# Kernel optimization log

Measured on AMD Instinct MI355X. Metric: run time of the kernel, lower is better.

The kernel has to match this reference:

```python
import jax, jax.numpy as jnp
import numpy as np

L, B, N, D, H, INTER = 4, 64, 128, 1024, 16, 4096
HD = D // H
EPS = 1e-12


def layer_norm(x, g, b):
    m = jnp.mean(x, axis=-1, keepdims=True)
    v = jnp.mean(jnp.square(x - m), axis=-1, keepdims=True)
    return (x - m) * jax.lax.rsqrt(v + EPS) * g + b


def fast_self_attention(x, wq_w, wq_b, wk_w, wk_b, hwq, hwk, tr_w, tr_b):
    # x: [B, T, D]
    Bq, T, _ = x.shape
    q = x @ wq_w + wq_b                                  # [B,T,D]
    hq = q.reshape(Bq, T, H, HD).transpose(0, 2, 1, 3)    # [B,H,T,hd]
    # additive attention over queries (mask scores are all-zero here)
    alpha = jax.nn.softmax(jnp.einsum('bhtd,hd->bht', hq, hwq) / np.sqrt(HD), axis=-1)
    gq = jnp.einsum('bht,bhtd->bhd', alpha, hq).reshape(Bq, 1, D)  # global query [B,1,D]
    k = x @ wk_w + wk_b
    p = k * gq                                            # [B,T,D]
    hp = p.reshape(Bq, T, H, HD).transpose(0, 2, 1, 3)
    beta = jax.nn.softmax(jnp.einsum('bhtd,hd->bht', hp, hwk) / np.sqrt(HD), axis=-1)
    gk = jnp.einsum('bht,bhtd->bhd', beta, hp).reshape(Bq, 1, D)   # global key [B,1,D]
    u = q * gk
    r = u @ tr_w + tr_b
    return r + q


def encoder_layer(x, p, i):
    a = fast_self_attention(x, p['wq_w'][i], p['wq_b'][i], p['wk_w'][i], p['wk_b'][i],
                            p['hwq'][i], p['hwk'][i], p['tr_w'][i], p['tr_b'][i])
    a = a @ p['so_w'][i] + p['so_b'][i]
    a = layer_norm(a, p['ln1_g'][i], p['ln1_b'][i])
    h = jax.nn.gelu(a @ p['int_w'][i] + p['int_b'][i], approximate=False)
    o = h @ p['out_w'][i] + p['out_b'][i]
    return layer_norm(o + a, p['ln2_g'][i], p['ln2_b'][i])


def setup_inputs() -> dict:
    key = jax.random.key(0)
    ks = iter(jax.random.split(key, 32))
    s = 0.02
    inp = {
        'x': jax.random.normal(next(ks), (B, N, D), jnp.float32),
        'wq_w': jax.random.normal(next(ks), (L, D, D)) * s,
        'wq_b': jnp.zeros((L, D)),
        'wk_w': jax.random.normal(next(ks), (L, D, D)) * s,
        'wk_b': jnp.zeros((L, D)),
        'hwq': jax.random.normal(next(ks), (L, H, HD)) * s,
        'hwk': jax.random.normal(next(ks), (L, H, HD)) * s,
        'tr_w': jax.random.normal(next(ks), (L, D, D)) * s,
        'tr_b': jnp.zeros((L, D)),
        'so_w': jax.random.normal(next(ks), (L, D, D)) * s,
        'so_b': jnp.zeros((L, D)),
        'ln1_g': jnp.ones((L, D)),
        'ln1_b': jnp.zeros((L, D)),
        'int_w': jax.random.normal(next(ks), (L, D, INTER)) * s,
        'int_b': jnp.zeros((L, INTER)),
        'out_w': jax.random.normal(next(ks), (L, INTER, D)) * s,
        'out_b': jnp.zeros((L, D)),
        'ln2_g': jnp.ones((L, D)),
        'ln2_b': jnp.zeros((L, D)),
        'pool_w': jax.random.normal(next(ks), (D, D)) * s,
        'pool_b': jnp.zeros((D,)),
        'pool_q': jax.random.normal(next(ks), (D,)) * s,
    }
    return inp


def reference(x, wq_w, wq_b, wk_w, wk_b, hwq, hwk, tr_w, tr_b, so_w, so_b,
              ln1_g, ln1_b, int_w, int_b, out_w, out_b, ln2_g, ln2_b,
              pool_w, pool_b, pool_q):
    p = dict(wq_w=wq_w, wq_b=wq_b, wk_w=wk_w, wk_b=wk_b, hwq=hwq, hwk=hwk,
             tr_w=tr_w, tr_b=tr_b, so_w=so_w, so_b=so_b, ln1_g=ln1_g, ln1_b=ln1_b,
             int_w=int_w, int_b=int_b, out_w=out_w, out_b=out_b, ln2_g=ln2_g, ln2_b=ln2_b)
    h = x
    for i in range(L):
        h = encoder_layer(h, p, i)
    # additive attention pooling (mask scores are zeros)
    scores = jnp.tanh(h @ pool_w + pool_b) @ pool_q       # [B,N]
    w = jax.nn.softmax(scores, axis=-1)
    return jnp.einsum('bn,bnd->bd', w, h)                 # [B,D]
```

## Files before the change

### kernel.cpp

```cpp
#include <hip/hip_runtime.h>
#include <hip/hip_bf16.h>
#include <math.h>

typedef unsigned short u16;
typedef __attribute__((ext_vector_type(4))) unsigned short u16x4;
typedef __attribute__((ext_vector_type(8))) unsigned short u16x8;
typedef __attribute__((ext_vector_type(8))) short s16x8;
typedef __attribute__((ext_vector_type(4))) float f32x4;

typedef const __attribute__((address_space(1))) void* gas_t;
typedef __attribute__((address_space(3))) void* las_t;

#define DI __device__ __forceinline__

static constexpr int Bc = 64, Nc = 128, Dc = 1024, Hc = 16, HDc = 64, Ic = 4096, Lc = 4;
static constexpr int Mrows = Bc * Nc;

DI float b2f(u16 u) { union { unsigned i; float f; } x; x.i = ((unsigned)u) << 16; return x.f; }
DI u16 f2b(float f) {
  union { float f; unsigned i; } x; x.f = f;
  unsigned r = x.i + 0x7FFF + ((x.i >> 16) & 1);
  return (u16)(r >> 16);
}

#define BARRIER do { asm volatile("" ::: "memory"); __builtin_amdgcn_s_barrier(); asm volatile("" ::: "memory"); } while (0)
#define VMC(N) asm volatile("s_waitcnt vmcnt(" #N ")" ::: "memory")

#define STG(PTR, ROW0, T, SLOT) do { \
    const u16* _s = (PTR) + (size_t)((ROW0) + srow) * K + (((T) << 6) + scol); \
    __builtin_amdgcn_global_load_lds((gas_t)_s, (las_t)(smem + (SLOT) + ldsw), 16, 0, 0); \
    __builtin_amdgcn_global_load_lds((gas_t)(_s + ((size_t)K << 3)), (las_t)(smem + (SLOT) + ldsw + 1024), 16, 0, 0); \
  } while (0)

#define LDA(BUFB, RH) do { \
    _Pragma("unroll") \
    for (int mi = 0; mi < 4; ++mi) { \
      af[mi][0] = *(const s16x8*)(smem + (BUFB) + Abase_rd + (RH) * 8192 + mi * 2048 + aoff0); \
      af[mi][1] = *(const s16x8*)(smem + (BUFB) + Abase_rd + (RH) * 8192 + mi * 2048 + aoff1); \
    } } while (0)

#define LDB(DST, BUFB, CH) do { \
    _Pragma("unroll") \
    for (int nj = 0; nj < 2; ++nj) { \
      DST[nj][0] = *(const s16x8*)(smem + (BUFB) + Bbase_rd + (CH) * 4096 + nj * 2048 + aoff0); \
      DST[nj][1] = *(const s16x8*)(smem + (BUFB) + Bbase_rd + (CH) * 4096 + nj * 2048 + aoff1); \
    } } while (0)

#define MFMAQ(RH, CH, BF) do { \
    __builtin_amdgcn_s_setprio(1); \
    _Pragma("unroll") \
    for (int kk = 0; kk < 2; ++kk) \
      _Pragma("unroll") \
      for (int mi = 0; mi < 4; ++mi) \
        _Pragma("unroll") \
        for (int nj = 0; nj < 2; ++nj) \
          acc[(RH) * 4 + mi][(CH) * 2 + nj] = __builtin_amdgcn_mfma_f32_16x16x32_bf16( \
              af[mi][kk], BF[nj][kk], acc[(RH) * 4 + mi][(CH) * 2 + nj], 0, 0, 0); \
    __builtin_amdgcn_s_setprio(0); \
  } while (0)

template <int EPI, bool SPLIT>
__global__ __launch_bounds__(512, 2) void gemm256(
    const u16* __restrict__ A, const u16* __restrict__ BT,
    const float* __restrict__ bias, const float* __restrict__ bias2,
    const u16* __restrict__ resid, u16* __restrict__ C, u16* __restrict__ C2,
    int M, int N, int K, int NC) {
  extern __shared__ __align__(16) char smem[];
  const int tid = threadIdx.x;
  const int l = tid & 63;
  const int w = tid >> 6;
  const int wr = w >> 2, wc = w & 3;

  const int GX = gridDim.x;
  int wg = blockIdx.y * GX + blockIdx.x;
  const int nwg = GX * gridDim.y;
  wg = (wg & 7) * (nwg >> 3) + (wg >> 3);
  const int bn0 = (wg % GX) * 256;
  const int bm0 = (wg / GX) * 256;

  const int NT = K >> 6;
  const int NI = NT >> 1;

  const int row_l = l & 15;
  const int kl = (l >> 4) * 8;
  const int xr = (row_l & 7) << 3;
  const int aoff0 = row_l * 128 + (((0 * 32 + kl) ^ xr) * 2);
  const int aoff1 = row_l * 128 + (((1 * 32 + kl) ^ xr) * 2);
  const int Abase_rd = wr * 16384;
  const int Bbase_rd = 32768 + (wc >> 1) * 16384 + (wc & 1) * 8192;

  const int srow = w * 16 + (l >> 3);
  const int scol = ((l & 7) ^ ((l >> 3) & 7)) << 3;
  const int ldsw = w * 2048;

  enum { b0A0 = 0, b0A1 = 16384, b0B0 = 32768, b0B1 = 49152,
         b1A0 = 65536, b1A1 = 81920, b1B0 = 98304, b1B1 = 114688 };

  STG(BT, bn0, 0, b0B0);
  STG(BT, bn0 + 128, 0, b0B1);
  STG(A, bm0, 0, b0A0);
  STG(A, bm0 + 128, 0, b0A1);
  STG(BT, bn0, 1, b1B0);
  STG(BT, bn0 + 128, 1, b1B1);
  VMC(4);
  BARRIER;

  f32x4 acc[8][4];
#pragma unroll
  for (int i = 0; i < 8; ++i)
#pragma unroll
    for (int j = 0; j < 4; ++j) acc[i][j] = f32x4{0.f, 0.f, 0.f, 0.f};
  s16x8 af[4][2], bf0[2][2], bf1[2][2];

  for (int j = 0; j < NI; ++j) {
    const int t1 = 2 * j + 1;
    int t2 = 2 * j + 2; if (t2 >= NT) t2 = 0;
    int t3 = 2 * j + 3; if (t3 >= NT) t3 = 1;
    LDA(0, 0); LDB(bf0, 0, 0);
    STG(A, bm0, t1, b1A0);
    BARRIER; MFMAQ(0, 0, bf0); BARRIER;
    LDB(bf1, 0, 1);
    STG(A, bm0 + 128, t1, b1A1);
    BARRIER; MFMAQ(0, 1, bf1); BARRIER;
    LDA(0, 1);
    STG(BT, bn0, t2, b0B0);
    BARRIER; MFMAQ(1, 0, bf0); BARRIER;
    STG(BT, bn0 + 128, t2, b0B1);
    STG(A, bm0, t2, b0A0);
    VMC(6);
    BARRIER; MFMAQ(1, 1, bf1); BARRIER;
    LDA(65536, 0); LDB(bf0, 65536, 0);
    STG(A, bm0 + 128, t2, b0A1);
    BARRIER; MFMAQ(0, 0, bf0); BARRIER;
    LDB(bf1, 65536, 1);
    BARRIER; MFMAQ(0, 1, bf1); BARRIER;
    LDA(65536, 1);
    STG(BT, bn0, t3, b1B0);
    BARRIER; MFMAQ(1, 0, bf0); BARRIER;
    STG(BT, bn0 + 128, t3, b1B1);
    VMC(4);
    BARRIER; MFMAQ(1, 1, bf1); BARRIER;
  }

  u16* Cout = C;
  const float* bi = bias;
  int cb = bn0;
  if (SPLIT) {
    const int half = N >> 1;
    if (bn0 >= half) { Cout = C2; bi = bias2; cb = bn0 - half; }
  }
  const int r0 = bm0 + wr * 128 + ((l >> 4) << 2);
#pragma unroll
  for (int fi = 0; fi < 8; ++fi) {
#pragma unroll
    for (int fj = 0; fj < 4; ++fj) {
      const int ocol = cb + wc * 64 + fj * 16 + (l & 15);
      const float bv = bi[ocol];
      const int row = r0 + fi * 16;
#pragma unroll
      for (int r = 0; r < 4; ++r) {
        float v = acc[fi][fj][r] + bv;
        if constexpr (EPI == 1) v += b2f(resid[(size_t)(row + r) * NC + ocol]);
        if constexpr (EPI == 2) v = 0.5f * v * (1.f + erff(v * 0.70710678118654752f));
        if constexpr (EPI == 3) v = tanhf(v);
        Cout[(size_t)(row + r) * NC + ocol] = f2b(v);
      }
    }
  }
}

#define LDA2(BUFB, RH) do { \
    _Pragma("unroll") \
    for (int mi = 0; mi < 2; ++mi) { \
      af[mi][0] = *(const s16x8*)(smem + (BUFB) + Abase_rd + ((RH) * 2 + mi) * 2048 + aoff0); \
      af[mi][1] = *(const s16x8*)(smem + (BUFB) + Abase_rd + ((RH) * 2 + mi) * 2048 + aoff1); \
    } } while (0)

#define MFMAQ2(RH, CH, BF) do { \
    __builtin_amdgcn_s_setprio(1); \
    _Pragma("unroll") \
    for (int kk = 0; kk < 2; ++kk) \
      _Pragma("unroll") \
      for (int mi = 0; mi < 2; ++mi) \
        _Pragma("unroll") \
        for (int nj = 0; nj < 2; ++nj) \
          acc[(RH) * 2 + mi][(CH) * 2 + nj] = __builtin_amdgcn_mfma_f32_16x16x32_bf16( \
              af[mi][kk], BF[nj][kk], acc[(RH) * 2 + mi][(CH) * 2 + nj], 0, 0, 0); \
    __builtin_amdgcn_s_setprio(0); \
  } while (0)

template <int EPI>
__global__ __launch_bounds__(512, 2) void gemm128n(
    const u16* __restrict__ A, const u16* __restrict__ BT,
    const float* __restrict__ bias, const u16* __restrict__ resid,
    u16* __restrict__ C, int M, int N, int K, int NC) {
  extern __shared__ __align__(16) char smem[];
  const int tid = threadIdx.x;
  const int l = tid & 63;
  const int w = tid >> 6;
  const int wr = w >> 1, wc = w & 1;

  const int GX = gridDim.x;
  int wg = blockIdx.y * GX + blockIdx.x;
  const int nwg = GX * gridDim.y;
  wg = (wg & 7) * (nwg >> 3) + (wg >> 3);
  const int bn0 = (wg % GX) * 128;
  const int bm0 = (wg / GX) * 256;

  const int NT = K >> 6;
  const int NI = NT >> 1;

  const int row_l = l & 15;
  const int kl = (l >> 4) * 8;
  const int xr = (row_l & 7) << 3;
  const int aoff0 = row_l * 128 + (((0 * 32 + kl) ^ xr) * 2);
  const int aoff1 = row_l * 128 + (((1 * 32 + kl) ^ xr) * 2);
  const int Abase_rd = (wr >> 1) * 16384 + (wr & 1) * 8192;
  const int Bbase_rd = 32768 + wc * 8192;

  const int srow = w * 16 + (l >> 3);
  const int scol = ((l & 7) ^ ((l >> 3) & 7)) << 3;
  const int ldsw = w * 2048;

  enum { c0A0 = 0, c0A1 = 16384, c0B = 32768,
         c1A0 = 49152, c1A1 = 65536, c1B = 81920 };

  STG(BT, bn0, 0, c0B);
  STG(A, bm0, 0, c0A0);
  STG(A, bm0 + 128, 0, c0A1);
  STG(BT, bn0, 1, c1B);
  VMC(2);
  BARRIER;

  f32x4 acc[4][4];
#pragma unroll
  for (int i = 0; i < 4; ++i)
#pragma unroll
    for (int j = 0; j < 4; ++j) acc[i][j] = f32x4{0.f, 0.f, 0.f, 0.f};
  s16x8 af[2][2], bf0[2][2], bf1[2][2];

  for (int j = 0; j < NI; ++j) {
    const int t1 = 2 * j + 1;
    int t2 = 2 * j + 2; if (t2 >= NT) t2 = 0;
    int t3 = 2 * j + 3; if (t3 >= NT) t3 = 1;
    LDA2(0, 0); LDB(bf0, 0, 0);
    STG(A, bm0, t1, c1A0);
    BARRIER; MFMAQ2(0, 0, bf0); BARRIER;
    LDB(bf1, 0, 1);
    STG(A, bm0 + 128, t1, c1A1);
    BARRIER; MFMAQ2(0, 1, bf1); BARRIER;
    LDA2(0, 1);
    STG(BT, bn0, t2, c0B);
    BARRIER; MFMAQ2(1, 0, bf0); BARRIER;
    STG(A, bm0, t2, c0A0);
    VMC(4);
    BARRIER; MFMAQ2(1, 1, bf1); BARRIER;
    LDA2(49152, 0); LDB(bf0, 49152, 0);
    STG(A, bm0 + 128, t2, c0A1);
    BARRIER; MFMAQ2(0, 0, bf0); BARRIER;
    LDB(bf1, 49152, 1);
    BARRIER; MFMAQ2(0, 1, bf1); BARRIER;
    LDA2(49152, 1);
    STG(BT, bn0, t3, c1B);
    BARRIER; MFMAQ2(1, 0, bf0); BARRIER;
    VMC(2);
    BARRIER; MFMAQ2(1, 1, bf1); BARRIER;
  }

  const int r0 = bm0 + wr * 64 + ((l >> 4) << 2);
#pragma unroll
  for (int fi = 0; fi < 4; ++fi) {
#pragma unroll
    for (int fj = 0; fj < 4; ++fj) {
      const int ocol = bn0 + wc * 64 + fj * 16 + (l & 15);
      const float bv = bias[ocol];
      const int row = r0 + fi * 16;
#pragma unroll
      for (int r = 0; r < 4; ++r) {
        float v = acc[fi][fj][r] + bv;
        if constexpr (EPI == 1) v += b2f(resid[(size_t)(row + r) * NC + ocol]);
        if constexpr (EPI == 2) v = 0.5f * v * (1.f + erff(v * 0.70710678118654752f));
        if constexpr (EPI == 3) v = tanhf(v);
        C[(size_t)(row + r) * NC + ocol] = f2b(v);
      }
    }
  }
}

DI void ttile(const float* in, u16* out, int R, int C, int r0, int c0, int t) {
  __shared__ u16 tile[32][33];
  const int lr = t >> 3;
  const int lc = (t & 7) * 4;
  f32x4 v = *(const f32x4*)(in + (size_t)(r0 + lr) * C + c0 + lc);
#pragma unroll
  for (int j = 0; j < 4; ++j) tile[lr][lc + j] = f2b(v[j]);
  __syncthreads();
  u16x4 o;
#pragma unroll
  for (int j = 0; j < 4; ++j) o[j] = tile[lc + j][lr];
  *(u16x4*)(out + (size_t)(c0 + lr) * R + r0 + lc) = o;
}

__global__ __launch_bounds__(256) void transpose_cvt(
    const float* __restrict__ in, u16* __restrict__ out, int R, int C) {
  ttile(in, out, R, C, blockIdx.y * 32, blockIdx.x * 32, threadIdx.x);
}

__global__ __launch_bounds__(256) void transpose4sq(
    const float* s0, const float* s1, const float* s2, const float* s3,
    u16* d0, u16* d1, u16* d2, u16* d3) {
  const int z = blockIdx.z;
  const float* in = z == 0 ? s0 : z == 1 ? s1 : z == 2 ? s2 : s3;
  u16* out = z == 0 ? d0 : z == 1 ? d1 : z == 2 ? d2 : d3;
  ttile(in, out, 1024, 1024, blockIdx.y * 32, blockIdx.x * 32, threadIdx.x);
}

__global__ __launch_bounds__(256) void transpose_io(
    const float* si, u16* di, const float* so, u16* dout) {
  if (blockIdx.z == 0) {
    ttile(si, di, 1024, 4096, blockIdx.y * 32, blockIdx.x * 32, threadIdx.x);
  } else {
    ttile(so, dout, 4096, 1024, blockIdx.x * 32, blockIdx.y * 32, threadIdx.x);
  }
}

__global__ __launch_bounds__(256) void cvt_k(
    const float* __restrict__ in, u16* __restrict__ out) {
  const size_t i = ((size_t)blockIdx.x * 256 + threadIdx.x) * 8;
  f32x4 a = *(const f32x4*)(in + i);
  f32x4 b = *(const f32x4*)(in + i + 4);
  u16x8 o;
#pragma unroll
  for (int j = 0; j < 4; ++j) o[j] = f2b(a[j]);
#pragma unroll
  for (int j = 0; j < 4; ++j) o[4 + j] = f2b(b[j]);
  *(u16x8*)(out + i) = o;
}

__global__ __launch_bounds__(128) void attn_gq(
    const u16* __restrict__ q, const float* __restrict__ hwq, float* __restrict__ gq) {
  const int bh = blockIdx.x;
  const int b = bh >> 4, h = bh & 15;
  const int tid = threadIdx.x;
  const int lane = tid & 63, wv = tid >> 6;
  __shared__ float hw[64];
  __shared__ float ex[128];
  __shared__ float part[64];
  __shared__ float xw[4];
  if (tid < 64) hw[tid] = hwq[h * 64 + tid];
  __syncthreads();
  const u16* row = q + ((size_t)(b * 128 + tid)) * Dc + h * 64;
  float s = 0.f;
#pragma unroll
  for (int c = 0; c < 8; ++c) {
    u16x8 v = *(const u16x8*)(row + c * 8);
#pragma unroll
    for (int j = 0; j < 8; ++j) s += b2f(v[j]) * hw[c * 8 + j];
  }
  s *= 0.125f;
  float m = s;
  for (int o = 32; o; o >>= 1) m = fmaxf(m, __shfl_xor(m, o));
  if (lane == 0) xw[wv] = m;
  __syncthreads();
  m = fmaxf(xw[0], xw[1]);
  const float e = __expf(s - m);
  ex[tid] = e;
  float sm = e;
  for (int o = 32; o; o >>= 1) sm += __shfl_xor(sm, o);
  if (lane == 0) xw[2 + wv] = sm;
  __syncthreads();
  const float sum = xw[2] + xw[3];
  const int d = tid & 63, half = tid >> 6;
  const u16* colp = q + ((size_t)(b * 128 + half * 64)) * Dc + h * 64 + d;
  float acc = 0.f;
  for (int t = 0; t < 64; ++t) acc += ex[half * 64 + t] * b2f(colp[(size_t)t * Dc]);
  if (half == 0) part[d] = acc;
  __syncthreads();
  if (half == 1) gq[b * Dc + h * 64 + d] = (part[d] + acc) / sum;
}

__global__ __launch_bounds__(128) void attn_gk(
    const u16* __restrict__ k, const float* __restrict__ hwk,
    const float* __restrict__ gq, float* __restrict__ gk) {
  const int bh = blockIdx.x;
  const int b = bh >> 4, h = bh & 15;
  const int tid = threadIdx.x;
  const int lane = tid & 63, wv = tid >> 6;
  __shared__ float hw[64];
  __shared__ float gqv[64];
  __shared__ float ex[128];
  __shared__ float part[64];
  __shared__ float xw[4];
  if (tid < 64) {
    hw[tid] = hwk[h * 64 + tid];
    gqv[tid] = gq[b * Dc + h * 64 + tid];
  }
  __syncthreads();
  const u16* row = k + ((size_t)(b * 128 + tid)) * Dc + h * 64;
  float s = 0.f;
#pragma unroll
  for (int c = 0; c < 8; ++c) {
    u16x8 v = *(const u16x8*)(row + c * 8);
#pragma unroll
    for (int j = 0; j < 8; ++j) s += b2f(v[j]) * gqv[c * 8 + j] * hw[c * 8 + j];
  }
  s *= 0.125f;
  float m = s;
  for (int o = 32; o; o >>= 1) m = fmaxf(m, __shfl_xor(m, o));
  if (lane == 0) xw[wv] = m;
  __syncthreads();
  m = fmaxf(xw[0], xw[1]);
  const float e = __expf(s - m);
  ex[tid] = e;
  float sm = e;
  for (int o = 32; o; o >>= 1) sm += __shfl_xor(sm, o);
  if (lane == 0) xw[2 + wv] = sm;
  __syncthreads();
  const float sum = xw[2] + xw[3];
  const int d = tid & 63, half = tid >> 6;
  const u16* colp = k + ((size_t)(b * 128 + half * 64)) * Dc + h * 64 + d;
  float acc = 0.f;
  for (int t = 0; t < 64; ++t) acc += ex[half * 64 + t] * b2f(colp[(size_t)t * Dc]);
  acc *= gqv[d];
  if (half == 0) part[d] = acc;
  __syncthreads();
  if (half == 1) gk[b * Dc + h * 64 + d] = (part[d] + acc) / sum;
}

__global__ __launch_bounds__(256) void mul_gk(
    const u16* __restrict__ q, const float* __restrict__ gk, u16* __restrict__ u) {
  const size_t i = ((size_t)blockIdx.x * 256 + threadIdx.x) * 8;
  const int col = (int)(i & (Dc - 1));
  const int b = (int)(i >> 17);
  u16x8 v = *(const u16x8*)(q + i);
  const float* g = gk + b * Dc + col;
  u16x8 o;
#pragma unroll
  for (int j = 0; j < 8; ++j) o[j] = f2b(b2f(v[j]) * g[j]);
  *(u16x8*)(u + i) = o;
}

__global__ __launch_bounds__(256) void ln_k(
    const u16* __restrict__ in, const float* __restrict__ g,
    const float* __restrict__ bta, u16* __restrict__ out) {
  const int row = blockIdx.x, tid = threadIdx.x;
  const int lane = tid & 63, wave = tid >> 6;
  __shared__ float red[8];
  const u16* p = in + (size_t)row * Dc + tid * 4;
  u16x4 v = *(const u16x4*)p;
  float x[4];
  float s = 0.f, sq = 0.f;
#pragma unroll
  for (int j = 0; j < 4; ++j) {
    x[j] = b2f(v[j]);
    s += x[j];
    sq += x[j] * x[j];
  }
  for (int o = 32; o; o >>= 1) {
    s += __shfl_down(s, o);
    sq += __shfl_down(sq, o);
  }
  if (lane == 0) {
    red[wave] = s;
    red[4 + wave] = sq;
  }
  __syncthreads();
  s = red[0] + red[1] + red[2] + red[3];
  sq = red[4] + red[5] + red[6] + red[7];
  const float mean = s * (1.f / 1024.f);
  const float var = sq * (1.f / 1024.f) - mean * mean;
  const float rs = rsqrtf(var + 1e-12f);
  f32x4 gv = *(const f32x4*)(g + tid * 4);
  f32x4 bv = *(const f32x4*)(bta + tid * 4);
  u16x4 o;
#pragma unroll
  for (int j = 0; j < 4; ++j) o[j] = f2b((x[j] - mean) * rs * gv[j] + bv[j]);
  *(u16x4*)(out + (size_t)row * Dc + tid * 4) = o;
}

__global__ __launch_bounds__(256) void pool_k(
    const u16* __restrict__ s1, const float* __restrict__ pq,
    const u16* __restrict__ h, float* __restrict__ out) {
  const int b = blockIdx.x, tid = threadIdx.x;
  __shared__ float pqs[1024];
  __shared__ float sc[128];
  __shared__ float ex[128];
  for (int i = tid; i < 1024; i += 256) pqs[i] = pq[i];
  __syncthreads();
  if (tid < 128) {
    const u16* row = s1 + ((size_t)(b * 128 + tid)) * Dc;
    float s = 0.f;
    for (int c = 0; c < 128; ++c) {
      u16x8 v = *(const u16x8*)(row + c * 8);
#pragma unroll
      for (int j = 0; j < 8; ++j) s += b2f(v[j]) * pqs[c * 8 + j];
    }
    sc[tid] = s;
  }
  __syncthreads();
  float m = -1e30f;
  for (int t = 0; t < 128; ++t) m = fmaxf(m, sc[t]);
  if (tid < 128) ex[tid] = __expf(sc[tid] - m);
  __syncthreads();
  float sum = 0.f;
  for (int t = 0; t < 128; ++t) sum += ex[t];
  const int d0 = tid * 4;
  float acc[4] = {0.f, 0.f, 0.f, 0.f};
  for (int n = 0; n < 128; ++n) {
    const float w = ex[n];
    u16x4 v = *(const u16x4*)(h + ((size_t)(b * 128 + n)) * Dc + d0);
#pragma unroll
    for (int j = 0; j < 4; ++j) acc[j] += w * b2f(v[j]);
  }
  const float inv = 1.f / sum;
  f32x4 o;
#pragma unroll
  for (int j = 0; j < 4; ++j) o[j] = acc[j] * inv;
  *(f32x4*)(out + b * Dc + d0) = o;
}

extern "C" void kernel_launch(void* const* d_in, const int* in_sizes, int n_in,
                              void* d_out, int out_size, void* d_ws, size_t ws_size,
                              hipStream_t stream) {
  const float* x = (const float*)d_in[0];
  const float* wq_w = (const float*)d_in[1];
  const float* wq_b = (const float*)d_in[2];
  const float* wk_w = (const float*)d_in[3];
  const float* wk_b = (const float*)d_in[4];
  const float* hwq = (const float*)d_in[5];
  const float* hwk = (const float*)d_in[6];
  const float* tr_w = (const float*)d_in[7];
  const float* tr_b = (const float*)d_in[8];
  const float* so_w = (const float*)d_in[9];
  const float* so_b = (const float*)d_in[10];
  const float* ln1g = (const float*)d_in[11];
  const float* ln1b = (const float*)d_in[12];
  const float* int_w = (const float*)d_in[13];
  const float* int_b = (const float*)d_in[14];
  const float* out_w = (const float*)d_in[15];
  const float* out_b = (const float*)d_in[16];
  const float* ln2g = (const float*)d_in[17];
  const float* ln2b = (const float*)d_in[18];
  const float* pool_w = (const float*)d_in[19];
  const float* pool_b = (const float*)d_in[20];
  const float* pool_q = (const float*)d_in[21];

  char* w = (char*)d_ws;
  auto alloc = [&](size_t bytes) {
    char* p = w;
    w += (bytes + 255) & ~(size_t)255;
    return p;
  };
  u16* wTqk = (u16*)alloc((size_t)2 * Dc * Dc * 2);
  u16* wTtr = (u16*)alloc((size_t)Dc * Dc * 2);
  u16* wTso = (u16*)alloc((size_t)Dc * Dc * 2);
  u16* wTint = (u16*)alloc((size_t)Dc * Ic * 2);
  u16* wTout = (u16*)alloc((size_t)Dc * Ic * 2);
  u16* wTpool = (u16*)alloc((size_t)Dc * Dc * 2);
  u16* qb = (u16*)alloc((size_t)Mrows * Dc * 2);
  u16* kb = (u16*)alloc((size_t)Mrows * Dc * 2);
  u16* ab = (u16*)alloc((size_t)Mrows * Dc * 2);
  u16* tb = (u16*)alloc((size_t)Mrows * Dc * 2);
  u16* xc = (u16*)alloc((size_t)Mrows * Dc * 2);
  u16* hb = (u16*)alloc((size_t)Mrows * Ic * 2);
  float* gqf = (float*)alloc((size_t)Bc * Dc * 4);
  float* gkf = (float*)alloc((size_t)Bc * Dc * 4);
  if ((size_t)(w - (char*)d_ws) > ws_size) return;

  static constexpr size_t LDSB = 131072;
  static constexpr size_t LDSB2 = 98304;
  hipFuncSetAttribute((const void*)gemm256<0, true>, hipFuncAttributeMaxDynamicSharedMemorySize, LDSB);
  hipFuncSetAttribute((const void*)gemm256<2, false>, hipFuncAttributeMaxDynamicSharedMemorySize, LDSB);
  hipFuncSetAttribute((const void*)gemm128n<0>, hipFuncAttributeMaxDynamicSharedMemorySize, LDSB2);
  hipFuncSetAttribute((const void*)gemm128n<1>, hipFuncAttributeMaxDynamicSharedMemorySize, LDSB2);
  hipFuncSetAttribute((const void*)gemm128n<3>, hipFuncAttributeMaxDynamicSharedMemorySize, LDSB2);

  const dim3 blk(256);
  const dim3 blkG(512);
  const dim3 gT1(Dc / 32, Dc / 32);
  const dim3 gT4(Dc / 32, Dc / 32, 4);
  const dim3 gTio(Ic / 32, Dc / 32, 2);
  const dim3 gQK(2048 / 256, Mrows / 256);
  const dim3 gNi(Ic / 256, Mrows / 256);
  const dim3 gO(Dc / 128, Mrows / 256);

  cvt_k<<<(Mrows * Dc) / (256 * 8), blk, 0, stream>>>(x, xc);

  for (int i = 0; i < Lc; ++i) {
    transpose4sq<<<gT4, blk, 0, stream>>>(
        wq_w + (size_t)i * Dc * Dc, wk_w + (size_t)i * Dc * Dc,
        tr_w + (size_t)i * Dc * Dc, so_w + (size_t)i * Dc * Dc,
        wTqk, wTqk + (size_t)Dc * Dc, wTtr, wTso);
    transpose_io<<<gTio, blk, 0, stream>>>(
        int_w + (size_t)i * Dc * Ic, wTint, out_w + (size_t)i * Ic * Dc, wTout);

    gemm256<0, true><<<gQK, blkG, LDSB, stream>>>(xc, wTqk, wq_b + i * Dc, wk_b + i * Dc,
                                                  nullptr, qb, kb, Mrows, 2048, Dc, Dc);
    attn_gq<<<Bc * Hc, 128, 0, stream>>>(qb, hwq + i * Hc * HDc, gqf);
    attn_gk<<<Bc * Hc, 128, 0, stream>>>(kb, hwk + i * Hc * HDc, gqf, gkf);
    mul_gk<<<(Mrows * Dc) / (256 * 8), blk, 0, stream>>>(qb, gkf, kb);
    gemm128n<1><<<gO, blkG, LDSB2, stream>>>(kb, wTtr, tr_b + i * Dc, qb, tb, Mrows, Dc, Dc, Dc);
    gemm128n<0><<<gO, blkG, LDSB2, stream>>>(tb, wTso, so_b + i * Dc, nullptr, kb, Mrows, Dc, Dc, Dc);
    ln_k<<<Mrows, blk, 0, stream>>>(kb, ln1g + i * Dc, ln1b + i * Dc, ab);
    gemm256<2, false><<<gNi, blkG, LDSB, stream>>>(ab, wTint, int_b + i * Ic, nullptr,
                                                   nullptr, hb, nullptr, Mrows, Ic, Dc, Ic);
    gemm128n<1><<<gO, blkG, LDSB2, stream>>>(hb, wTout, out_b + i * Dc, ab, tb, Mrows, Dc, Ic, Dc);
    ln_k<<<Mrows, blk, 0, stream>>>(tb, ln2g + i * Dc, ln2b + i * Dc, xc);
  }

  transpose_cvt<<<gT1, blk, 0, stream>>>(pool_w, wTpool, Dc, Dc);
  gemm128n<3><<<gO, blkG, LDSB2, stream>>>(xc, wTpool, pool_b, nullptr, tb, Mrows, Dc, Dc, Dc);
  pool_k<<<Bc, blk, 0, stream>>>(tb, pool_q, xc, (float*)d_out);
}
```

Before: 1.267 ms.

## Add 128x128 square-tile GEMM with two blocks per CU for intermediate projection

Adds a new 256-thread GEMM kernel with 128x128 output tiles, double-buffered LDS (64KB) and launch bounds allowing two workgroups per CU. It replaces the 256x256 tile, 512-thread kernel for the GELU intermediate projection (M=8192, N=4096, K=1024). The smaller tiles give four times more workgroups and higher occupancy, which helps hide latency and improves load balance. In exchange each tile reuses loaded data less, so global and LDS traffic per FLOP goes up.

```diff
diff --git a/kernel.cpp b/kernel.cpp
--- a/kernel.cpp
+++ b/kernel.cpp
@@ -287,6 +287,128 @@
   }
 }
 
+#define LDA3(DST, BUFB, RH) do { \
+    _Pragma("unroll") \
+    for (int mi = 0; mi < 2; ++mi) { \
+      DST[mi][0] = *(const s16x8*)(smem + (BUFB) + Abase_rd + ((RH) * 2 + mi) * 2048 + aoff0); \
+      DST[mi][1] = *(const s16x8*)(smem + (BUFB) + Abase_rd + ((RH) * 2 + mi) * 2048 + aoff1); \
+    } } while (0)
+
+#define MFMAQ3(RH, CH, AF, BF) do { \
+    __builtin_amdgcn_s_setprio(1); \
+    _Pragma("unroll") \
+    for (int kk = 0; kk < 2; ++kk) \
+      _Pragma("unroll") \
+      for (int mi = 0; mi < 2; ++mi) \
+        _Pragma("unroll") \
+        for (int nj = 0; nj < 2; ++nj) \
+          acc[(RH) * 2 + mi][(CH) * 2 + nj] = __builtin_amdgcn_mfma_f32_16x16x32_bf16( \
+              AF[mi][kk], BF[nj][kk], acc[(RH) * 2 + mi][(CH) * 2 + nj], 0, 0, 0); \
+    __builtin_amdgcn_s_setprio(0); \
+  } while (0)
+
+template <int EPI>
+__global__ __launch_bounds__(256, 2) void gemm128sq(
+    const u16* __restrict__ A, const u16* __restrict__ BT,
+    const float* __restrict__ bias, const u16* __restrict__ resid,
+    u16* __restrict__ C, int M, int N, int K, int NC) {
+  extern __shared__ __align__(16) char smem[];
+  const int tid = threadIdx.x;
+  const int l = tid & 63;
+  const int w = tid >> 6;
+  const int wr = w >> 1, wc = w & 1;
+
+  const int GX = gridDim.x;
+  int wg = blockIdx.y * GX + blockIdx.x;
+  const int nwg = GX * gridDim.y;
+  wg = (wg & 7) * (nwg >> 3) + (wg >> 3);
+  const int bn0 = (wg % GX) * 128;
+  const int bm0 = (wg / GX) * 128;
+
+  const int NT = K >> 6;
+  const int NI = NT >> 1;
+
+  const int row_l = l & 15;
+  const int kl = (l >> 4) * 8;
+  const int xr = (row_l & 7) << 3;
+  const int aoff0 = row_l * 128 + (((0 * 32 + kl) ^ xr) * 2);
+  const int aoff1 = row_l * 128 + (((1 * 32 + kl) ^ xr) * 2);
+  const int Abase_rd = wr * 8192;
+  const int Bbase_rd = 16384 + wc * 8192;
+
+  const int srow = w * 16 + (l >> 3);
+  const int scol = ((l & 7) ^ ((l >> 3) & 7)) << 3;
+  const int ldsw = w * 2048;
+
+  enum { d0A0 = 0, d0A1 = 8192, d0B0 = 16384, d0B1 = 24576,
+         d1A0 = 32768, d1A1 = 40960, d1B0 = 49152, d1B1 = 57344 };
+
+  STG(A, bm0, 0, d0A0);
+  STG(A, bm0 + 64, 0, d0A1);
+  STG(BT, bn0, 0, d0B0);
+  STG(BT, bn0 + 64, 0, d0B1);
+  STG(BT, bn0, 1, d1B0);
+  STG(BT, bn0 + 64, 1, d1B1);
+  VMC(4);
+  BARRIER;
+
+  f32x4 acc[4][4];
+#pragma unroll
+  for (int i = 0; i < 4; ++i)
+#pragma unroll
+    for (int j = 0; j < 4; ++j) acc[i][j] = f32x4{0.f, 0.f, 0.f, 0.f};
+  s16x8 af[2][2], ag[2][2], bf0[2][2], bf1[2][2];
+
+  for (int j = 0; j < NI; ++j) {
+    const int t1 = 2 * j + 1;
+    int t2 = 2 * j + 2; if (t2 >= NT) t2 = 0;
+    int t3 = 2 * j + 3; if (t3 >= NT) t3 = 1;
+    LDA3(af, 0, 0); LDB(bf0, 0, 0);
+    STG(A, bm0, t1, d1A0);
+    BARRIER; MFMAQ3(0, 0, af, bf0); BARRIER;
+    LDB(bf1, 0, 1);
+    STG(A, bm0 + 64, t1, d1A1);
+    BARRIER; MFMAQ3(0, 1, af, bf1); BARRIER;
+    LDA3(ag, 0, 1);
+    STG(BT, bn0, t2, d0B0);
+    BARRIER; MFMAQ3(1, 0, ag, bf0); BARRIER;
+    STG(BT, bn0 + 64, t2, d0B1);
+    VMC(4);
+    BARRIER; MFMAQ3(1, 1, ag, bf1); BARRIER;
+    LDA3(af, 32768, 0); LDB(bf0, 32768, 0);
+    STG(A, bm0, t2, d0A0);
+    BARRIER; MFMAQ3(0, 0, af, bf0); BARRIER;
+    LDB(bf1, 32768, 1);
+    STG(A, bm0 + 64, t2, d0A1);
+    BARRIER; MFMAQ3(0, 1, af, bf1); BARRIER;
+    LDA3(ag, 32768, 1);
+    STG(BT, bn0, t3, d1B0);
+    BARRIER; MFMAQ3(1, 0, ag, bf0); BARRIER;
+    STG(BT, bn0 + 64, t3, d1B1);
+    VMC(4);
+    BARRIER; MFMAQ3(1, 1, ag, bf1); BARRIER;
+  }
+
+  const int r0 = bm0 + wr * 64 + ((l >> 4) << 2);
+#pragma unroll
+  for (int fi = 0; fi < 4; ++fi) {
+#pragma unroll
+    for (int fj = 0; fj < 4; ++fj) {
+      const int ocol = bn0 + wc * 64 + fj * 16 + (l & 15);
+      const float bv = bias[ocol];
+      const int row = r0 + fi * 16;
+#pragma unroll
+      for (int r = 0; r < 4; ++r) {
+        float v = acc[fi][fj][r] + bv;
+        if constexpr (EPI == 1) v += b2f(resid[(size_t)(row + r) * NC + ocol]);
+        if constexpr (EPI == 2) v = 0.5f * v * (1.f + erff(v * 0.70710678118654752f));
+        if constexpr (EPI == 3) v = tanhf(v);
+        C[(size_t)(row + r) * NC + ocol] = f2b(v);
+      }
+    }
+  }
+}
+
 DI void ttile(const float* in, u16* out, int R, int C, int r0, int c0, int t) {
   __shared__ u16 tile[32][33];
   const int lr = t >> 3;
@@ -569,11 +691,12 @@
 
   static constexpr size_t LDSB = 131072;
   static constexpr size_t LDSB2 = 98304;
+  static constexpr size_t LDSB3 = 65536;
   hipFuncSetAttribute((const void*)gemm256<0, true>, hipFuncAttributeMaxDynamicSharedMemorySize, LDSB);
-  hipFuncSetAttribute((const void*)gemm256<2, false>, hipFuncAttributeMaxDynamicSharedMemorySize, LDSB);
   hipFuncSetAttribute((const void*)gemm128n<0>, hipFuncAttributeMaxDynamicSharedMemorySize, LDSB2);
   hipFuncSetAttribute((const void*)gemm128n<1>, hipFuncAttributeMaxDynamicSharedMemorySize, LDSB2);
   hipFuncSetAttribute((const void*)gemm128n<3>, hipFuncAttributeMaxDynamicSharedMemorySize, LDSB2);
+  hipFuncSetAttribute((const void*)gemm128sq<2>, hipFuncAttributeMaxDynamicSharedMemorySize, LDSB3);
 
   const dim3 blk(256);
   const dim3 blkG(512);
@@ -581,7 +704,7 @@
   const dim3 gT4(Dc / 32, Dc / 32, 4);
   const dim3 gTio(Ic / 32, Dc / 32, 2);
   const dim3 gQK(2048 / 256, Mrows / 256);
-  const dim3 gNi(Ic / 256, Mrows / 256);
+  const dim3 gI(Ic / 128, Mrows / 128);
   const dim3 gO(Dc / 128, Mrows / 256);
 
   cvt_k<<<(Mrows * Dc) / (256 * 8), blk, 0, stream>>>(x, xc);
@@ -602,8 +725,8 @@
     gemm128n<1><<<gO, blkG, LDSB2, stream>>>(kb, wTtr, tr_b + i * Dc, qb, tb, Mrows, Dc, Dc, Dc);
     gemm128n<0><<<gO, blkG, LDSB2, stream>>>(tb, wTso, so_b + i * Dc, nullptr, kb, Mrows, Dc, Dc, Dc);
     ln_k<<<Mrows, blk, 0, stream>>>(kb, ln1g + i * Dc, ln1b + i * Dc, ab);
-    gemm256<2, false><<<gNi, blkG, LDSB, stream>>>(ab, wTint, int_b + i * Ic, nullptr,
-                                                   nullptr, hb, nullptr, Mrows, Ic, Dc, Ic);
+    gemm128sq<2><<<gI, blk, LDSB3, stream>>>(ab, wTint, int_b + i * Ic, nullptr,
+                                             hb, Mrows, Ic, Dc, Ic);
     gemm128n<1><<<gO, blkG, LDSB2, stream>>>(hb, wTout, out_b + i * Dc, ab, tb, Mrows, Dc, Ic, Dc);
     ln_k<<<Mrows, blk, 0, stream>>>(tb, ln2g + i * Dc, ln2b + i * Dc, xc);
   }
```

New measurement: 1.308 ms. 1.03x slower.
